# Performance work log

Measured on AMD Instinct MI355X. Metric: run time of the kernel, lower is better.

The kernel has to match this reference:

```python
import jax, jax.numpy as jnp
import numpy as np

GROUP = 32  # quantization group size along K, fixed by the call site


def setup_inputs() -> dict:
    key = jax.random.key(0)
    k1, k2, k3 = jax.random.split(key, 3)
    M, K, N = 1, 8192, 16384
    A = jax.random.normal(k1, (M, K), dtype=jnp.float16)
    # packed int4 weights: each byte holds two nibbles -> [N, K//2]
    B = jax.random.randint(k2, (N, K // 2), 0, 256, dtype=jnp.int32)
    scalesAndZeros = (jax.random.normal(k3, (N, K // GROUP, 2), dtype=jnp.float16))
    return {"A": A, "B": B, "scalesAndZeros": scalesAndZeros}


def _dequant(B, scalesAndZeros):
    # B: [N, K//2] bytes, two int4 values per byte (low nibble = even k)
    N, Kh = B.shape
    K = Kh * 2
    low = B & 0xF
    high = (B >> 4) & 0xF
    q = jnp.stack([low, high], axis=-1).reshape(N, K).astype(jnp.float32) - 8.0
    scales = scalesAndZeros[..., 0].astype(jnp.float32)  # [N, K//GROUP]
    zeros = scalesAndZeros[..., 1].astype(jnp.float32)   # [N, K//GROUP]
    qg = q.reshape(N, K // GROUP, GROUP)
    W = qg * scales[:, :, None] + zeros[:, :, None]       # [N, K//GROUP, GROUP]
    return W.reshape(N, K)


def reference(A, B, scalesAndZeros):
    # int4 weight-only quantized GEMV: out[m, n] = sum_k A[m, k] * dequant(W)[n, k]
    W = _dequant(B, scalesAndZeros)                        # [N, K] fp32
    out = jnp.einsum("mk,nk->mn", A.astype(jnp.float32), W)
    return out.astype(A.dtype)                             # [1, N] fp16
```

## Files before the change

### kernel.cpp

```cpp
#include <hip/hip_runtime.h>
#include <hip/hip_bf16.h>


#define ROWS 8

__global__ __launch_bounds__(256) void gemv_w4p(
    const float4* __restrict__ A4,
    const int4*   __restrict__ B,
    const float2* __restrict__ SZ,
    float* __restrict__ out,
    int N)
{
    const int t  = threadIdx.x;
    const int n0 = blockIdx.x * ROWS;

    float a[4][8];
    float sAj[4];
#pragma unroll
    for (int j = 0; j < 4; ++j) {
        const float4 x = A4[2 * t + 512 * j];
        const float4 y = A4[2 * t + 512 * j + 1];
        a[j][0] = x.x; a[j][1] = x.y; a[j][2] = x.z; a[j][3] = x.w;
        a[j][4] = y.x; a[j][5] = y.y; a[j][6] = y.z; a[j][7] = y.w;
        sAj[j] = ((x.x + x.y) + (x.z + x.w)) + ((y.x + y.y) + (y.z + y.w));
    }

    const int4*   Bp = B  + (size_t)n0 * 1024 + t;
    const float2* Sp = SZ + (size_t)n0 * 256 + (t >> 2);

    float acc[ROWS];
#pragma unroll
    for (int r = 0; r < ROWS; ++r) acc[r] = 0.0f;

    int4 b[ROWS];
#pragma unroll
    for (int r = 0; r < ROWS; ++r) b[r] = Bp[1024 * r];

#pragma unroll
    for (int j = 0; j < 4; ++j) {
        int4 bn[ROWS];
        if (j < 3) {
#pragma unroll
            for (int r = 0; r < ROWS; ++r) bn[r] = Bp[1024 * r + 256 * (j + 1)];
        }

        float2 szv[ROWS];
#pragma unroll
        for (int r = 0; r < ROWS; ++r) szv[r] = Sp[256 * r + 64 * j];

#pragma unroll
        for (int r = 0; r < ROWS; ++r) {
            const int bb[4] = { b[r].x, b[r].y, b[r].z, b[r].w };
            float dot = 0.0f;
#pragma unroll
            for (int m = 0; m < 4; ++m) {
                dot = fmaf(a[j][2 * m],     (float)(bb[m] & 0xF),        dot);
                dot = fmaf(a[j][2 * m + 1], (float)((bb[m] >> 4) & 0xF), dot);
            }
            const float s  = szv[r].x;
            const float zz = fmaf(-8.0f, s, szv[r].y);
            acc[r] = fmaf(s, dot, acc[r]);
            acc[r] = fmaf(zz, sAj[j], acc[r]);
        }

        if (j < 3) {
#pragma unroll
            for (int r = 0; r < ROWS; ++r) b[r] = bn[r];
        }
    }

    __shared__ float red[ROWS][4];
    const int lane = t & 63;
    const int w    = t >> 6;
#pragma unroll
    for (int r = 0; r < ROWS; ++r) {
        float v = acc[r];
#pragma unroll
        for (int off = 32; off > 0; off >>= 1)
            v += __shfl_down(v, off, 64);
        if (lane == 0) red[r][w] = v;
    }
    __syncthreads();
    if (t < ROWS) {
        const int n = n0 + t;
        if (n < N)
            out[n] = (red[t][0] + red[t][1]) + (red[t][2] + red[t][3]);
    }
}

extern "C" void kernel_launch(void* const* d_in, const int* in_sizes, int n_in,
                              void* d_out, int out_size, void* d_ws, size_t ws_size,
                              hipStream_t stream) {
    const float4* A4 = (const float4*)d_in[0];
    const int4*   B  = (const int4*)d_in[1];
    const float2* SZ = (const float2*)d_in[2];
    float* out = (float*)d_out;

    const int N = out_size;
    gemv_w4p<<<N / ROWS, 256, 0, stream>>>(A4, B, SZ, out, N);
}
```

Baseline: 375.6 us.

## Use 512-thread blocks, stage scales in LDS, issue all B loads upfront

Doubles the threads per block to 512 so each thread covers two K chunks instead of four. The block's scale/zero data is loaded cooperatively into shared memory with coalesced accesses before a barrier. All 16 int4 weight loads per thread are issued at once instead of being double-buffered. The goal is more memory-level parallelism and better coalescing of scale reads. The cost is an extra barrier, 16KB of LDS per block, and higher register pressure under the occupancy hint.

```diff
diff --git a/kernel.cpp b/kernel.cpp
--- a/kernel.cpp
+++ b/kernel.cpp
@@ -3,8 +3,9 @@
 
 
 #define ROWS 8
+#define TPB  512
 
-__global__ __launch_bounds__(256) void gemv_w4p(
+__global__ __launch_bounds__(TPB, 4) void gemv_w4s(
     const float4* __restrict__ A4,
     const int4*   __restrict__ B,
     const float2* __restrict__ SZ,
@@ -14,62 +15,64 @@
     const int t  = threadIdx.x;
     const int n0 = blockIdx.x * ROWS;
 
-    float a[4][8];
-    float sAj[4];
+    __shared__ float2 sz_s[ROWS * 256];
+    __shared__ float  red[ROWS][8];
+
+    float a[2][8];
+    float sAj[2];
 #pragma unroll
-    for (int j = 0; j < 4; ++j) {
-        const float4 x = A4[2 * t + 512 * j];
-        const float4 y = A4[2 * t + 512 * j + 1];
+    for (int j = 0; j < 2; ++j) {
+        const int i = t + 512 * j;
+        const float4 x = A4[2 * i];
+        const float4 y = A4[2 * i + 1];
         a[j][0] = x.x; a[j][1] = x.y; a[j][2] = x.z; a[j][3] = x.w;
         a[j][4] = y.x; a[j][5] = y.y; a[j][6] = y.z; a[j][7] = y.w;
         sAj[j] = ((x.x + x.y) + (x.z + x.w)) + ((y.x + y.y) + (y.z + y.w));
     }
 
-    const int4*   Bp = B  + (size_t)n0 * 1024 + t;
-    const float2* Sp = SZ + (size_t)n0 * 256 + (t >> 2);
+    {
+        const float2* Sp = SZ + (size_t)n0 * 256;
+#pragma unroll
+        for (int q = 0; q < 4; ++q) {
+            const int idx = t + TPB * q;
+            sz_s[idx] = Sp[idx];
+        }
+    }
+    __syncthreads();
 
+    const int4* Bp = B + (size_t)n0 * 1024 + t;
+    int4 b[ROWS][2];
+#pragma unroll
+    for (int r = 0; r < ROWS; ++r) {
+#pragma unroll
+        for (int j = 0; j < 2; ++j)
+            b[r][j] = Bp[1024 * r + 512 * j];
+    }
+
+    const int g0 = t >> 2;
     float acc[ROWS];
 #pragma unroll
     for (int r = 0; r < ROWS; ++r) acc[r] = 0.0f;
 
-    int4 b[ROWS];
 #pragma unroll
-    for (int r = 0; r < ROWS; ++r) b[r] = Bp[1024 * r];
-
+    for (int r = 0; r < ROWS; ++r) {
 #pragma unroll
-    for (int j = 0; j < 4; ++j) {
-        int4 bn[ROWS];
-        if (j < 3) {
-#pragma unroll
-            for (int r = 0; r < ROWS; ++r) bn[r] = Bp[1024 * r + 256 * (j + 1)];
-        }
-
-        float2 szv[ROWS];
-#pragma unroll
-        for (int r = 0; r < ROWS; ++r) szv[r] = Sp[256 * r + 64 * j];
-
-#pragma unroll
-        for (int r = 0; r < ROWS; ++r) {
-            const int bb[4] = { b[r].x, b[r].y, b[r].z, b[r].w };
+        for (int j = 0; j < 2; ++j) {
+            const float2 sz = sz_s[r * 256 + g0 + 128 * j];
+            const int bb[4] = { b[r][j].x, b[r][j].y, b[r][j].z, b[r][j].w };
             float dot = 0.0f;
 #pragma unroll
             for (int m = 0; m < 4; ++m) {
                 dot = fmaf(a[j][2 * m],     (float)(bb[m] & 0xF),        dot);
                 dot = fmaf(a[j][2 * m + 1], (float)((bb[m] >> 4) & 0xF), dot);
             }
-            const float s  = szv[r].x;
-            const float zz = fmaf(-8.0f, s, szv[r].y);
+            const float s  = sz.x;
+            const float zz = fmaf(-8.0f, s, sz.y);
             acc[r] = fmaf(s, dot, acc[r]);
             acc[r] = fmaf(zz, sAj[j], acc[r]);
         }
-
-        if (j < 3) {
-#pragma unroll
-            for (int r = 0; r < ROWS; ++r) b[r] = bn[r];
-        }
     }
 
-    __shared__ float red[ROWS][4];
     const int lane = t & 63;
     const int w    = t >> 6;
 #pragma unroll
@@ -83,8 +86,12 @@
     __syncthreads();
     if (t < ROWS) {
         const int n = n0 + t;
-        if (n < N)
-            out[n] = (red[t][0] + red[t][1]) + (red[t][2] + red[t][3]);
+        if (n < N) {
+            float v = 0.0f;
+#pragma unroll
+            for (int w2 = 0; w2 < 8; ++w2) v += red[t][w2];
+            out[n] = v;
+        }
     }
 }
 
@@ -97,5 +104,5 @@
     float* out = (float*)d_out;
 
     const int N = out_size;
-    gemv_w4p<<<N / ROWS, 256, 0, stream>>>(A4, B, SZ, out, N);
+    gemv_w4s<<<N / ROWS, TPB, 0, stream>>>(A4, B, SZ, out, N);
 }
```

New measurement: 370.9 us. About the same (-1.2%).
